# Performance work log

Hardware: AMD Instinct MI355X
Metric: run time of the kernel (lower is better)

Reference implementation:

```python
import jax, jax.numpy as jnp
import numpy as np

D_MODEL = 1024
NUM_HEADS = 16
D_K = D_MODEL // NUM_HEADS
B, S = 4, 2048
NEG_INF = -1.0e9  # matches torch masked_fill value


def setup_inputs() -> dict:
    key = jax.random.key(0)
    ks = jax.random.split(key, 6)
    scale = 1.0 / np.sqrt(D_MODEL)
    x = jax.random.normal(ks[0], (B, S, D_MODEL), dtype=jnp.float32)
    # causal mask, broadcast over batch and heads: [1,1,S,S]
    mask = jnp.tril(jnp.ones((S, S), dtype=jnp.int32))[None, None]
    Wq = jax.random.normal(ks[1], (D_MODEL, D_MODEL), dtype=jnp.float32) * scale
    Wk = jax.random.normal(ks[2], (D_MODEL, D_MODEL), dtype=jnp.float32) * scale
    Wv = jax.random.normal(ks[3], (D_MODEL, D_MODEL), dtype=jnp.float32) * scale
    Wo = jax.random.normal(ks[4], (D_MODEL, D_MODEL), dtype=jnp.float32) * scale
    bq = jnp.zeros((D_MODEL,), jnp.float32)
    bk = jnp.zeros((D_MODEL,), jnp.float32)
    bv = jnp.zeros((D_MODEL,), jnp.float32)
    bo = jnp.zeros((D_MODEL,), jnp.float32)
    return {"x": x, "mask": mask, "Wq": Wq, "bq": bq, "Wk": Wk, "bk": bk,
            "Wv": Wv, "bv": bv, "Wo": Wo, "bo": bo}


def reference(x, mask, Wq, bq, Wk, bk, Wv, bv, Wo, bo):
    b, s, d = x.shape
    # projections (torch Linear: y = x @ W.T + b)
    q = (x @ Wq.T + bq).reshape(b, s, NUM_HEADS, D_K).transpose(0, 2, 1, 3)  # [B,H,S,Dk]
    k = (x @ Wk.T + bk).reshape(b, s, NUM_HEADS, D_K).transpose(0, 2, 1, 3)
    v = (x @ Wv.T + bv).reshape(b, s, NUM_HEADS, D_K).transpose(0, 2, 1, 3)
    scores = jnp.einsum("bhqd,bhkd->bhqk", q, k) / jnp.sqrt(jnp.float32(D_K))
    scores = jnp.where(mask == 0, NEG_INF, scores)
    attn = jax.nn.softmax(scores, axis=-1)
    out = jnp.einsum("bhqk,bhkd->bhqd", attn, v)  # [B,H,S,Dk]
    out = out.transpose(0, 2, 1, 3).reshape(b, s, d)
    return out @ Wo.T + bo
```

## Files before the change

kernel.cpp:

```cpp
#include <hip/hip_runtime.h>
#include <hip/hip_bf16.h>

#define D_MODEL 1024
#define NUM_HEADS 16
#define DK 64
#define BATCH 4
#define SEQ 2048

typedef __hip_bfloat16 bf16;
typedef __attribute__((ext_vector_type(8))) short bf16x8;
typedef __attribute__((ext_vector_type(4))) short bf16x4;
typedef __attribute__((ext_vector_type(4))) float f32x4;

typedef __attribute__((address_space(1))) const unsigned int gu32;
typedef __attribute__((address_space(3))) unsigned int lu32;

#define QSCALE (0.125f * 1.44269504089f)

#define FENCE asm volatile("" ::: "memory")
#define BAR_OPEN()  do { FENCE; __builtin_amdgcn_s_barrier();              \
    asm volatile("s_waitcnt lgkmcnt(0)" ::: "memory");                     \
    __builtin_amdgcn_sched_barrier(0); } while (0)
#define BAR_CLOSE() do { FENCE; __builtin_amdgcn_s_barrier(); FENCE; } while (0)

__device__ __forceinline__ void gll16(const bf16* g, bf16* l) {
    __builtin_amdgcn_global_load_lds((gu32*)g, (lu32*)l, 16, 0, 0);
}

__device__ __forceinline__ bf16x8 frag_ld(const bf16* lds, int row, int h, int quad) {
    return *(const bf16x8*)(lds + row * 64 + (((h << 2) + quad) ^ (row & 7)) * 8);
}

__global__ __launch_bounds__(256)
void cvt_bf16(const float* __restrict__ x,  const float* __restrict__ Wq,
              const float* __restrict__ Wk, const float* __restrict__ Wv,
              const float* __restrict__ Wo, bf16* __restrict__ xb,
              bf16* __restrict__ Wb)
{
    size_t v = (size_t)blockIdx.x * 256 + threadIdx.x;
    size_t e = v * 4;
    const float* src; bf16* dst; size_t off;
    if (e < 8388608) { src = x; dst = xb; off = e; }
    else {
        size_t r = e - 8388608;
        int w = (int)(r >> 20);
        off = r & 1048575;
        src = (w == 0) ? Wq : (w == 1) ? Wk : (w == 2) ? Wv : Wo;
        dst = Wb + ((size_t)w << 20);
    }
    float4 f = *(const float4*)(src + off);
    bf16 o[4] = {__float2bfloat16(f.x), __float2bfloat16(f.y),
                 __float2bfloat16(f.z), __float2bfloat16(f.w)};
    *(bf16x4*)(dst + off) = *(const bf16x4*)o;
}

template<int MODE>
__global__ __launch_bounds__(512, 1)
void gemm_pipe(const bf16* __restrict__ A, const bf16* __restrict__ W,
               const float* __restrict__ bqv, const float* __restrict__ bkv,
               const float* __restrict__ bvv,
               bf16* __restrict__ Q, bf16* __restrict__ Kt, bf16* __restrict__ Vtr,
               float* __restrict__ fout)
{
    __shared__ bf16 lds[65536];

    const int t = threadIdx.x;
    const int wave = t >> 6, lane = t & 63;
    const int quad = lane >> 4, l16 = lane & 15;
    const int wm = wave >> 2, wn = wave & 3;

    const int colb = blockIdx.x;
    const int rowBase = blockIdx.y * 256;

    const bf16* Ablk = A + (size_t)rowBase * 1024;
    const bf16* Bblk = W + (MODE == 1 ? ((size_t)3 << 20) : (size_t)0)
                         + (size_t)colb * 256 * 1024;

    auto stageAhalf = [&](int d, int h, int k0) {
        bf16* dst = (bf16*)lds + d * 16384 + h * 8192;
        #pragma unroll
        for (int p = 0; p < 2; ++p) {
            int idx = t + p * 512;
            int row = idx >> 3, cg = (idx & 7) ^ (row & 7);
            gll16(Ablk + (size_t)(h * 128 + row) * 1024 + k0 + cg * 8, dst + idx * 8);
        }
    };
    auto stageBhalf = [&](int d, int h, int k0) {
        bf16* dst = (bf16*)lds + 32768 + d * 16384 + h * 8192;
        #pragma unroll
        for (int p = 0; p < 2; ++p) {
            int idx = t + p * 512;
            int row = idx >> 3, cg = (idx & 7) ^ (row & 7);
            gll16(Bblk + (size_t)(h * 128 + row) * 1024 + k0 + cg * 8, dst + idx * 8);
        }
    };

    f32x4 acc[8][4];
    #pragma unroll
    for (int mf = 0; mf < 8; ++mf)
        #pragma unroll
        for (int nf = 0; nf < 4; ++nf) acc[mf][nf] = (f32x4){0.f, 0.f, 0.f, 0.f};

    const bf16* Aha = (const bf16*)lds + wm * 8192;
    const bf16* Ahb = (const bf16*)lds + 16384 + wm * 8192;
    const bf16* Bha = (const bf16*)lds + 32768 + (wn >> 1) * 8192;
    const bf16* Bhb = (const bf16*)lds + 49152 + (wn >> 1) * 8192;
    const int brow0 = (wn & 1) * 64;

    auto rdA4 = [&](bf16x8 (&f)[4][2], const bf16* Ah, int mh) {
        #pragma unroll
        for (int m4 = 0; m4 < 4; ++m4)
            #pragma unroll
            for (int kk = 0; kk < 2; ++kk)
                f[m4][kk] = frag_ld(Ah, mh * 64 + m4 * 16 + l16, kk, quad);
    };
    auto rdB2 = [&](bf16x8 (&f)[2][2], const bf16* Bh, int nh) {
        #pragma unroll
        for (int n2 = 0; n2 < 2; ++n2)
            #pragma unroll
            for (int kk = 0; kk < 2; ++kk)
                f[n2][kk] = frag_ld(Bh, brow0 + nh * 32 + n2 * 16 + l16, kk, quad);
    };
    auto mfma16 = [&](bf16x8 (&af)[4][2], bf16x8 (&bfr)[2][2], int mh, int nh) {
        __builtin_amdgcn_s_setprio(1);
        #pragma unroll
        for (int kk = 0; kk < 2; ++kk)
            #pragma unroll
            for (int m4 = 0; m4 < 4; ++m4)
                #pragma unroll
                for (int n2 = 0; n2 < 2; ++n2)
                    acc[mh * 4 + m4][nh * 2 + n2] =
                        __builtin_amdgcn_mfma_f32_16x16x32_bf16(
                            af[m4][kk], bfr[n2][kk], acc[mh * 4 + m4][nh * 2 + n2],
                            0, 0, 0);
        __builtin_amdgcn_s_setprio(0);
    };

    stageBhalf(0, 0, 0);  stageBhalf(0, 1, 0);
    stageAhalf(0, 0, 0);  stageAhalf(0, 1, 0);
    stageBhalf(1, 0, 64); stageBhalf(1, 1, 64);
    stageAhalf(1, 0, 64); stageAhalf(1, 1, 64);
    asm volatile("s_waitcnt vmcnt(8)" ::: "memory");
    FENCE; __builtin_amdgcn_s_barrier(); FENCE;

    for (int it = 0; it < 8; ++it) {
        const bool more = (it < 7);
        const int ka2 = it * 128 + 128, kb2 = ka2 + 64;
        bf16x8 aX[4][2], aY[4][2], bX[2][2], bY[2][2];

        rdA4(aX, Aha, 0); rdB2(bX, Bha, 0);
        asm volatile("s_waitcnt lgkmcnt(8)" ::: "memory");
        BAR_OPEN(); mfma16(aX, bX, 0, 0); BAR_CLOSE();

        rdB2(bY, Bha, 1);
        BAR_OPEN(); mfma16(aX, bY, 0, 1); BAR_CLOSE();

        rdA4(aY, Aha, 1);
        if (more) stageBhalf(0, 0, ka2);
        BAR_OPEN(); mfma16(aY, bY, 1, 1); BAR_CLOSE();

        if (more) stageBhalf(0, 1, ka2);
        BAR_OPEN(); mfma16(aY, bX, 1, 0);
        if (more) asm volatile("s_waitcnt vmcnt(4)" ::: "memory");
        else      asm volatile("s_waitcnt vmcnt(0)" ::: "memory");
        BAR_CLOSE();

        rdA4(aX, Ahb, 0); rdB2(bX, Bhb, 0);
        if (more) stageAhalf(0, 0, ka2);
        asm volatile("s_waitcnt lgkmcnt(8)" ::: "memory");
        BAR_OPEN(); mfma16(aX, bX, 0, 0); BAR_CLOSE();

        rdB2(bY, Bhb, 1);
        if (more) stageAhalf(0, 1, ka2);
        BAR_OPEN(); mfma16(aX, bY, 0, 1); BAR_CLOSE();

        rdA4(aY, Ahb, 1);
        if (more) { stageBhalf(1, 0, kb2); stageBhalf(1, 1, kb2); }
        BAR_OPEN(); mfma16(aY, bY, 1, 1); BAR_CLOSE();

        if (more) { stageAhalf(1, 0, kb2); stageAhalf(1, 1, kb2); }
        BAR_OPEN(); mfma16(aY, bX, 1, 0);
        if (more) {
            asm volatile("s_waitcnt vmcnt(8)" ::: "memory");
            BAR_CLOSE();
        }
    }

    if (MODE == 0) {
        const int proj = colb >> 2;
        const float* bias = proj == 0 ? bqv : (proj == 1 ? bkv : bvv);
        const int cb = (colb & 3) * 256;
        float bias4[4];
        #pragma unroll
        for (int nf = 0; nf < 4; ++nf)
            bias4[nf] = bias[cb + wn * 64 + nf * 16 + l16];
        const float oscale = proj == 0 ? QSCALE : 1.0f;
        #pragma unroll
        for (int mf = 0; mf < 8; ++mf)
            #pragma unroll
            for (int rr = 0; rr < 4; ++rr) {
                int r = rowBase + wm * 128 + mf * 16 + quad * 4 + rr;
                int b_ = r >> 11, s_ = r & 2047;
                #pragma unroll
                for (int nf = 0; nf < 4; ++nf) {
                    int c = cb + wn * 64 + nf * 16 + l16;
                    float v = (acc[mf][nf][rr] + bias4[nf]) * oscale;
                    int h_ = c >> 6, d_ = c & 63;
                    size_t bh = (size_t)(b_ * NUM_HEADS + h_);
                    if (proj == 2)
                        Vtr[(bh * DK + d_) * SEQ + s_] = __float2bfloat16(v);
                    else {
                        bf16* dst = proj == 0 ? Q : Kt;
                        dst[(bh * SEQ + s_) * DK + d_] = __float2bfloat16(v);
                    }
                }
            }
    } else {
        #pragma unroll
        for (int mf = 0; mf < 8; ++mf)
            #pragma unroll
            for (int rr = 0; rr < 4; ++rr) {
                int r = rowBase + wm * 128 + mf * 16 + quad * 4 + rr;
                #pragma unroll
                for (int nf = 0; nf < 4; ++nf) {
                    int c = colb * 256 + wn * 64 + nf * 16 + l16;
                    fout[(size_t)r * 1024 + c] = acc[mf][nf][rr] + bqv[c];
                }
            }
    }
}

#define AS 72

__device__ __forceinline__ void stage_attn(const bf16* __restrict__ Kb,
                                           const bf16* __restrict__ Vb,
                                           int k0, bf16* ks, bf16* vs, int t)
{
    #pragma unroll
    for (int p = 0; p < 2; ++p) {
        int idx = t + p * 256;
        int row = idx >> 3, cl = idx & 7;
        int cg = cl ^ (row & 7);
        gll16(Kb + (size_t)(k0 + row) * DK + cg * 8, ks + idx * 8);
        gll16(Vb + (size_t)row * SEQ + k0 + cg * 8, vs + idx * 8);
    }
}

__global__ __launch_bounds__(256)
void attn_mfma(const bf16* __restrict__ Q, const bf16* __restrict__ K,
               const bf16* __restrict__ Vt, bf16* __restrict__ ctx)
{
    __shared__ bf16 Ks[2][64 * 64];
    __shared__ bf16 Vs[2][64 * 64];
    __shared__ bf16 Ps[4][2][16 * AS];

    const int t    = threadIdx.x;
    const int wave = t >> 6, lane = t & 63;
    const int quad = lane >> 4, l16 = lane & 15;
    const int bh   = blockIdx.x;
    const int qbi  = 15 - blockIdx.y;
    const int b_ = bh >> 4, h_ = bh & 15;

    const bf16* Qb = Q  + (size_t)bh * SEQ * DK;
    const bf16* Kb = K  + (size_t)bh * SEQ * DK;
    const bf16* Vb = Vt + (size_t)bh * DK * SEQ;

    const int qb  = qbi * 128;
    const int ntiles = 2 * qbi + 2;

    bf16x8 qf[2][2];
    #pragma unroll
    for (int i = 0; i < 2; ++i) {
        const int qrow = qb + wave * 32 + i * 16 + l16;
        qf[i][0] = *(const bf16x8*)(Qb + (size_t)qrow * DK + quad * 8);
        qf[i][1] = *(const bf16x8*)(Qb + (size_t)qrow * DK + 32 + quad * 8);
    }

    f32x4 O[2][4];
    float lsum[2][4];
    #pragma unroll
    for (int i = 0; i < 2; ++i)
        #pragma unroll
        for (int nc = 0; nc < 4; ++nc) {
            O[i][nc] = (f32x4){0.f, 0.f, 0.f, 0.f};
            lsum[i][nc] = 0.f;
        }

    stage_attn(Kb, Vb, 0, Ks[0], Vs[0], t);
    __syncthreads();

    for (int kt = 0; kt < ntiles; ++kt) {
        const int cur = kt & 1;
        const int k0  = kt * 64;
        if (kt + 1 < ntiles)
            stage_attn(Kb, Vb, k0 + 64, Ks[cur ^ 1], Vs[cur ^ 1], t);

        const bool diag = (kt + 2 >= ntiles);
        const bool skip = (kt == ntiles - 1) && (wave < 2);

        if (!skip) {
            bf16x8 kf[4][2];
            #pragma unroll
            for (int h = 0; h < 4; ++h) {
                kf[h][0] = frag_ld(Ks[cur], h * 16 + l16, 0, quad);
                kf[h][1] = frag_ld(Ks[cur], h * 16 + l16, 1, quad);
            }

            #pragma unroll
            for (int i = 0; i < 2; ++i) {
                const int qrow0i = qb + wave * 32 + i * 16;
                float lacc[4];
                #pragma unroll
                for (int r = 0; r < 4; ++r) lacc[r] = lsum[i][r];
                #pragma unroll
                for (int h = 0; h < 4; ++h) {
                    f32x4 a = (f32x4){0.f, 0.f, 0.f, 0.f};
                    a = __builtin_amdgcn_mfma_f32_16x16x32_bf16(qf[i][0], kf[h][0], a, 0, 0, 0);
                    a = __builtin_amdgcn_mfma_f32_16x16x32_bf16(qf[i][1], kf[h][1], a, 0, 0, 0);
                    #pragma unroll
                    for (int r = 0; r < 4; ++r) {
                        float ss = a[r];
                        if (diag && (k0 + h * 16 + l16 > qrow0i + quad * 4 + r))
                            ss = -1e30f;
                        float p = exp2f(ss);
                        lacc[r] += p;
                        Ps[wave][i][(quad * 4 + r) * AS + h * 16 + l16] =
                            __float2bfloat16(p);
                    }
                }
                #pragma unroll
                for (int r = 0; r < 4; ++r) lsum[i][r] = lacc[r];
            }

            bf16x8 pf[2][2];
            #pragma unroll
            for (int i = 0; i < 2; ++i) {
                pf[i][0] = *(const bf16x8*)(&Ps[wave][i][l16 * AS + quad * 8]);
                pf[i][1] = *(const bf16x8*)(&Ps[wave][i][l16 * AS + 32 + quad * 8]);
            }
            __builtin_amdgcn_s_setprio(1);
            #pragma unroll
            for (int nc = 0; nc < 4; ++nc) {
                bf16x8 vf0 = frag_ld(Vs[cur], nc * 16 + l16, 0, quad);
                bf16x8 vf1 = frag_ld(Vs[cur], nc * 16 + l16, 1, quad);
                #pragma unroll
                for (int i = 0; i < 2; ++i) {
                    O[i][nc] = __builtin_amdgcn_mfma_f32_16x16x32_bf16(pf[i][0], vf0, O[i][nc], 0, 0, 0);
                    O[i][nc] = __builtin_amdgcn_mfma_f32_16x16x32_bf16(pf[i][1], vf1, O[i][nc], 0, 0, 0);
                }
            }
            __builtin_amdgcn_s_setprio(0);
        }
        __syncthreads();
    }

    #pragma unroll
    for (int i = 0; i < 2; ++i) {
        #pragma unroll
        for (int r = 0; r < 4; ++r) {
            #pragma unroll
            for (int off = 1; off < 16; off <<= 1)
                lsum[i][r] += __shfl_xor(lsum[i][r], off, 64);
        }
        #pragma unroll
        for (int nc = 0; nc < 4; ++nc)
            #pragma unroll
            for (int r = 0; r < 4; ++r) {
                const int row = qb + wave * 32 + i * 16 + quad * 4 + r;
                float v = O[i][nc][r] / lsum[i][r];
                ctx[((size_t)(b_ * SEQ + row)) * D_MODEL + h_ * DK + nc * 16 + l16] =
                    __float2bfloat16(v);
            }
    }
}

extern "C" void kernel_launch(void* const* d_in, const int* in_sizes, int n_in,
                              void* d_out, int out_size, void* d_ws, size_t ws_size,
                              hipStream_t stream) {
    const float* x  = (const float*)d_in[0];
    const float* Wq = (const float*)d_in[2];
    const float* bq = (const float*)d_in[3];
    const float* Wk = (const float*)d_in[4];
    const float* bk = (const float*)d_in[5];
    const float* Wv = (const float*)d_in[6];
    const float* bv = (const float*)d_in[7];
    const float* Wo = (const float*)d_in[8];
    const float* bo = (const float*)d_in[9];
    float* out = (float*)d_out;

    const size_t per = (size_t)BATCH * NUM_HEADS * SEQ * DK;
    bf16* Q   = (bf16*)d_ws;
    bf16* Kt  = Q  + per;
    bf16* Vtr = Kt + per;
    bf16* xb  = Vtr + per;
    bf16* ctx = xb;
    bf16* Wb  = xb + per;

    hipLaunchKernelGGL(cvt_bf16, dim3(12288), dim3(256), 0, stream,
                       x, Wq, Wk, Wv, Wo, xb, Wb);

    hipLaunchKernelGGL((gemm_pipe<0>), dim3(12, 32), dim3(512), 0, stream,
                       xb, Wb, bq, bk, bv, Q, Kt, Vtr, (float*)nullptr);

    hipLaunchKernelGGL(attn_mfma, dim3(64, 16), dim3(256), 0,
                       stream, Q, Kt, Vtr, ctx);

    hipLaunchKernelGGL((gemm_pipe<1>), dim3(4, 32), dim3(512), 0, stream,
                       ctx, Wb, bo, (const float*)nullptr, (const float*)nullptr,
                       (bf16*)nullptr, (bf16*)nullptr, (bf16*)nullptr, out);
}
```

Baseline: 304.8 us.

## Replace output projection GEMM with smaller-tile kernel to fill all CUs

Splits the templated GEMM into a dedicated QKV kernel and a new output-projection kernel using 128x128 tiles and 256-thread blocks. This gives 512 blocks instead of 128 so every compute unit has work. The new kernel is simpler and single-buffered, giving up the deep software pipeline of the original. The attention epilogue also multiplies by a hardware reciprocal instead of dividing by the row sum.

```diff
diff --git a/kernel.cpp b/kernel.cpp
--- a/kernel.cpp
+++ b/kernel.cpp
@@ -54,13 +54,11 @@
     *(bf16x4*)(dst + off) = *(const bf16x4*)o;
 }
 
-template<int MODE>
 __global__ __launch_bounds__(512, 1)
-void gemm_pipe(const bf16* __restrict__ A, const bf16* __restrict__ W,
-               const float* __restrict__ bqv, const float* __restrict__ bkv,
-               const float* __restrict__ bvv,
-               bf16* __restrict__ Q, bf16* __restrict__ Kt, bf16* __restrict__ Vtr,
-               float* __restrict__ fout)
+void gemm_qkv(const bf16* __restrict__ A, const bf16* __restrict__ W,
+              const float* __restrict__ bqv, const float* __restrict__ bkv,
+              const float* __restrict__ bvv,
+              bf16* __restrict__ Q, bf16* __restrict__ Kt, bf16* __restrict__ Vtr)
 {
     __shared__ bf16 lds[65536];
 
@@ -73,8 +71,7 @@
     const int rowBase = blockIdx.y * 256;
 
     const bf16* Ablk = A + (size_t)rowBase * 1024;
-    const bf16* Bblk = W + (MODE == 1 ? ((size_t)3 << 20) : (size_t)0)
-                         + (size_t)colb * 256 * 1024;
+    const bf16* Bblk = W + (size_t)colb * 256 * 1024;
 
     auto stageAhalf = [&](int d, int h, int k0) {
         bf16* dst = (bf16*)lds + d * 16384 + h * 8192;
@@ -186,7 +183,7 @@
         }
     }
 
-    if (MODE == 0) {
+    {
         const int proj = colb >> 2;
         const float* bias = proj == 0 ? bqv : (proj == 1 ? bkv : bvv);
         const int cb = (colb & 3) * 256;
@@ -215,19 +212,82 @@
                     }
                 }
             }
-    } else {
-        #pragma unroll
-        for (int mf = 0; mf < 8; ++mf)
-            #pragma unroll
-            for (int rr = 0; rr < 4; ++rr) {
-                int r = rowBase + wm * 128 + mf * 16 + quad * 4 + rr;
-                #pragma unroll
-                for (int nf = 0; nf < 4; ++nf) {
-                    int c = colb * 256 + wn * 64 + nf * 16 + l16;
-                    fout[(size_t)r * 1024 + c] = acc[mf][nf][rr] + bqv[c];
-                }
-            }
-    }
+    }
+}
+
+__device__ __forceinline__ void stage_gll128(const bf16* __restrict__ src,
+                                             bf16* lds, int t, int k0)
+{
+    #pragma unroll
+    for (int p = 0; p < 4; ++p) {
+        int idx = t + p * 256;
+        int row = idx >> 3, cl = idx & 7;
+        int cg = cl ^ (row & 7);
+        gll16(src + (size_t)row * 1024 + k0 + cg * 8, lds + idx * 8);
+    }
+}
+
+__global__ __launch_bounds__(256)
+void gemm_out(const bf16* __restrict__ ctx, const bf16* __restrict__ Wb,
+              const float* __restrict__ bo, float* __restrict__ out)
+{
+    __shared__ bf16 As[128 * 64];
+    __shared__ bf16 Bs[128 * 64];
+    const int t = threadIdx.x;
+    const int wave = t >> 6, lane = t & 63;
+    const int quad = lane >> 4, l16 = lane & 15;
+    const int wr = wave >> 1, wc = wave & 1;
+    const int colBase = blockIdx.x * 128;
+    const int rowBase = blockIdx.y * 128;
+
+    const bf16* Ablk = ctx + (size_t)rowBase * 1024;
+    const bf16* Bblk = Wb + ((size_t)3 << 20) + (size_t)colBase * 1024;
+
+    f32x4 acc[4][4];
+    #pragma unroll
+    for (int i = 0; i < 4; ++i)
+        #pragma unroll
+        for (int j = 0; j < 4; ++j) acc[i][j] = (f32x4){0.f, 0.f, 0.f, 0.f};
+
+    for (int k0 = 0; k0 < 1024; k0 += 64) {
+        stage_gll128(Ablk, As, t, k0);
+        stage_gll128(Bblk, Bs, t, k0);
+        __syncthreads();
+        #pragma unroll
+        for (int h = 0; h < 2; ++h) {
+            bf16x8 af[4], bfr[4];
+            #pragma unroll
+            for (int i = 0; i < 4; ++i)
+                af[i] = frag_ld(As, wr * 64 + i * 16 + l16, h, quad);
+            #pragma unroll
+            for (int j = 0; j < 4; ++j)
+                bfr[j] = frag_ld(Bs, wc * 64 + j * 16 + l16, h, quad);
+            #pragma unroll
+            for (int i = 0; i < 4; ++i)
+                #pragma unroll
+                for (int j = 0; j < 4; ++j)
+                    acc[i][j] = __builtin_amdgcn_mfma_f32_16x16x32_bf16(af[i], bfr[j],
+                                                                        acc[i][j], 0, 0, 0);
+        }
+        __syncthreads();
+    }
+
+    float bias4[4];
+    #pragma unroll
+    for (int j = 0; j < 4; ++j)
+        bias4[j] = bo[colBase + wc * 64 + j * 16 + l16];
+
+    #pragma unroll
+    for (int i = 0; i < 4; ++i)
+        #pragma unroll
+        for (int rr = 0; rr < 4; ++rr) {
+            int r = rowBase + wr * 64 + i * 16 + quad * 4 + rr;
+            #pragma unroll
+            for (int j = 0; j < 4; ++j) {
+                int c = colBase + wc * 64 + j * 16 + l16;
+                out[(size_t)r * 1024 + c] = acc[i][j][rr] + bias4[j];
+            }
+        }
 }
 
 #define AS 72
@@ -356,18 +416,20 @@
 
     #pragma unroll
     for (int i = 0; i < 2; ++i) {
+        float inv[4];
         #pragma unroll
         for (int r = 0; r < 4; ++r) {
             #pragma unroll
             for (int off = 1; off < 16; off <<= 1)
                 lsum[i][r] += __shfl_xor(lsum[i][r], off, 64);
+            inv[r] = __builtin_amdgcn_rcpf(lsum[i][r]);
         }
         #pragma unroll
         for (int nc = 0; nc < 4; ++nc)
             #pragma unroll
             for (int r = 0; r < 4; ++r) {
                 const int row = qb + wave * 32 + i * 16 + quad * 4 + r;
-                float v = O[i][nc][r] / lsum[i][r];
+                float v = O[i][nc][r] * inv[r];
                 ctx[((size_t)(b_ * SEQ + row)) * D_MODEL + h_ * DK + nc * 16 + l16] =
                     __float2bfloat16(v);
             }
@@ -399,13 +461,12 @@
     hipLaunchKernelGGL(cvt_bf16, dim3(12288), dim3(256), 0, stream,
                        x, Wq, Wk, Wv, Wo, xb, Wb);
 
-    hipLaunchKernelGGL((gemm_pipe<0>), dim3(12, 32), dim3(512), 0, stream,
-                       xb, Wb, bq, bk, bv, Q, Kt, Vtr, (float*)nullptr);
+    hipLaunchKernelGGL(gemm_qkv, dim3(12, 32), dim3(512), 0, stream,
+                       xb, Wb, bq, bk, bv, Q, Kt, Vtr);
 
     hipLaunchKernelGGL(attn_mfma, dim3(64, 16), dim3(256), 0,
                        stream, Q, Kt, Vtr, ctx);
 
-    hipLaunchKernelGGL((gemm_pipe<1>), dim3(4, 32), dim3(512), 0, stream,
-                       ctx, Wb, bo, (const float*)nullptr, (const float*)nullptr,
-                       (bf16*)nullptr, (bf16*)nullptr, (bf16*)nullptr, out);
-}
+    hipLaunchKernelGGL(gemm_out, dim3(8, 64), dim3(256), 0, stream,
+                       ctx, Wb, bo, out);
+}
```

New measurement: 299.9 us. About the same (-1.6%).
